# Kernel optimization log

Measured on AMD Instinct MI355X. Metric: run time of the kernel, lower is better.

Reference implementation:

```python
import jax, jax.numpy as jnp
import numpy as np

IN_CHANNELS = 256
OUT_CHANNELS = 256
KERNEL_SIZE = 3
CHANNELS_PER_FILTER = 32
B, H, W = 4, 56, 56


def setup_inputs() -> dict:
    key = jax.random.key(0)
    k1, k2, k3 = jax.random.split(key, 3)
    x = jax.random.normal(k1, (B, IN_CHANNELS, H, W), dtype=jnp.float32)
    # kaiming-uniform-ish scale: bound = 1/sqrt(fan_in)
    fan_in = CHANNELS_PER_FILTER * KERNEL_SIZE ** 2
    bound = 1.0 / np.sqrt(fan_in)
    weight = jax.random.uniform(
        k2, (OUT_CHANNELS, CHANNELS_PER_FILTER, KERNEL_SIZE, KERNEL_SIZE),
        dtype=jnp.float32, minval=-bound, maxval=bound)
    connections = jax.random.randint(
        k3, (OUT_CHANNELS, CHANNELS_PER_FILTER), 0, IN_CHANNELS, dtype=jnp.int32)
    return {"x": x, "weight": weight, "connections": connections}


def reference(x, weight, connections):
    # x: (B, Cin, H, W); weight: (O, cpf, k, k); connections: (O, cpf) int32
    B_, O, cpf = x.shape[0], weight.shape[0], weight.shape[1]
    Hh, Ww = x.shape[2], x.shape[3]
    # Gather each filter's input-channel subset: (B, O, cpf, H, W)
    gathered = x[:, connections]
    # Grouped conv: each of the O groups convolves its cpf channels.
    gathered = gathered.reshape(B_, O * cpf, Hh, Ww)
    out = jax.lax.conv_general_dilated(
        gathered, weight,
        window_strides=(1, 1), padding="SAME",
        dimension_numbers=("NCHW", "OIHW", "NCHW"),
        feature_group_count=O)
    return out  # (B, O, H, W)
```

## Files before the change

kernel.cpp:

```cpp
#include <hip/hip_runtime.h>
#include <stdint.h>

#define NPIX 3136
#define OC 256
#define IC 256
#define CPF 32
#define BUF_FLOATS 3456
#define ZROW 3360

typedef const __attribute__((address_space(1))) uint32_t* gptr_t;
typedef __attribute__((address_space(3))) uint32_t* lptr_t;

__device__ __forceinline__ float dpp_shr1(float v) {
    return __int_as_float(__builtin_amdgcn_update_dpp(
        0, __float_as_int(v), 0x111, 0xF, 0xF, true));
}
__device__ __forceinline__ float dpp_shl1(float v) {
    return __int_as_float(__builtin_amdgcn_update_dpp(
        0, __float_as_int(v), 0x101, 0xF, 0xF, true));
}

__global__ __launch_bounds__(256, 4) void sparse_conv_kernel(
    const float* __restrict__ x, const float* __restrict__ weight,
    const int* __restrict__ connections, float* __restrict__ out)
{
    __shared__ __align__(16) float buf[2][BUF_FLOATS];
    __shared__ __align__(16) float wlds[CPF * 12];
    __shared__ int clds[CPF];

    const int bid = blockIdx.x;
    const int b = bid & 3;
    const int o = bid >> 2;
    const int t = threadIdx.x;
    const int lane = t & 63;
    const int wv = t >> 6;

    if (t < 64) { buf[0][ZROW + t] = 0.f; buf[1][ZROW + t] = 0.f; }

    {
        const float* wo = weight + o * CPF * 9;
        for (int i = t; i < CPF * 9; i += 256) {
            int c = i / 9, k = i - c * 9;
            wlds[c * 12 + k] = wo[i];
        }
        if (t < CPF) clds[t] = connections[o * CPF + t];
    }

    const int cbase = (wv == 0) ? 0 : (3 * wv + 1);
    const int cnum  = (wv == 0) ? 4 : 3;
    int goffs[4], coffs[4];
#pragma unroll
    for (int i = 0; i < 4; ++i) {
        const int chunk = cbase + i;
        int go = chunk * 256 + lane * 4;
        goffs[i] = (go > 3132) ? 3132 : go;
        coffs[i] = chunk * 256;
    }

    const float* xb = x + (size_t)b * IC * NPIX;
    const int s = t & 15;
    const int g = t >> 4;
    const bool active = (g < 14);

    int ro[6];
#pragma unroll
    for (int k = 0; k < 6; ++k) {
        const int rr = 4 * g - 1 + k;
        ro[k] = (((unsigned)rr < 56u) ? rr * 56 : ZROW) + 4 * s;
    }

    float4 acc[4];
#pragma unroll
    for (int r = 0; r < 4; ++r) acc[r] = make_float4(0.f, 0.f, 0.f, 0.f);

    __syncthreads();

    auto dma = [&](int c, float* dst) {
        const float* plane = xb + (size_t)clds[c] * NPIX;
        for (int i = 0; i < cnum; ++i)
            __builtin_amdgcn_global_load_lds((gptr_t)(plane + goffs[i]),
                                             (lptr_t)(dst + coffs[i]), 16, 0, 0);
    };

    auto compute = [&](const float* base, int c) {
        const float4* wp = reinterpret_cast<const float4*>(&wlds[c * 12]);
        const float4 wa = wp[0], wb = wp[1], wc = wp[2];
        const float wt[9] = {wa.x, wa.y, wa.z, wa.w, wb.x, wb.y, wb.z, wb.w, wc.x};
        if (active) {
#pragma unroll
            for (int k = 0; k < 6; ++k) {
                const float4 m = *reinterpret_cast<const float4*>(base + ro[k]);
                const float L = dpp_shr1(m.w);
                float       R = dpp_shl1(m.x);
                R = (s == 13) ? 0.f : R;
#pragma unroll
                for (int r = 0; r < 4; ++r) {
                    const int kh = k - r;
                    if (kh >= 0 && kh < 3) {
                        const float w0 = wt[kh * 3 + 0];
                        const float w1 = wt[kh * 3 + 1];
                        const float w2 = wt[kh * 3 + 2];
                        acc[r].x += w0 * L    + w1 * m.x + w2 * m.y;
                        acc[r].y += w0 * m.x  + w1 * m.y + w2 * m.z;
                        acc[r].z += w0 * m.y  + w1 * m.z + w2 * m.w;
                        acc[r].w += w0 * m.z  + w1 * m.w + w2 * R;
                    }
                }
            }
        }
    };

    dma(0, &buf[0][0]);
    __syncthreads();

#pragma unroll 1
    for (int it = 0; it < 16; ++it) {
        const int c = 2 * it;
        dma(c + 1, &buf[1][0]);
        compute(&buf[0][0], c);
        __syncthreads();
        if (it < 15) dma(c + 2, &buf[0][0]);
        compute(&buf[1][0], c + 1);
        __syncthreads();
    }

    if (active && s < 14) {
        float* ob = out + ((size_t)b * OC + o) * NPIX + (4 * g) * 56 + 4 * s;
#pragma unroll
        for (int r = 0; r < 4; ++r)
            *reinterpret_cast<float4*>(ob + r * 56) = acc[r];
    }
}

extern "C" void kernel_launch(void* const* d_in, const int* in_sizes, int n_in,
                              void* d_out, int out_size, void* d_ws, size_t ws_size,
                              hipStream_t stream) {
    const float* x    = (const float*)d_in[0];
    const float* wgt  = (const float*)d_in[1];
    const int*   conn = (const int*)d_in[2];
    float* out = (float*)d_out;

    dim3 grid(4 * OC);
    dim3 block(256);
    hipLaunchKernelGGL(sparse_conv_kernel, grid, block, 0, stream, x, wgt, conn, out);
}
```

Measured before the change: 122.2 us.

## Split each output plane into two row halves to double blocks and occupancy

Each block now computes half of an output plane (28 rows), so the grid doubles to 2048 blocks and LDS per block shrinks, allowing launch bounds of 8 blocks per CU. Each thread computes 2 output rows instead of 4, with a 29-row halo window loaded per channel. Weights and connection indices are read directly from global memory instead of being staged in LDS. The aim is more parallelism and latency hiding, at the cost of extra halo loads (29 of 56 rows per half) and less per-thread reuse of loaded rows.

```diff
diff --git a/kernel.cpp b/kernel.cpp
--- a/kernel.cpp
+++ b/kernel.cpp
@@ -5,8 +5,10 @@
 #define OC 256
 #define IC 256
 #define CPF 32
-#define BUF_FLOATS 3456
-#define ZROW 3360
+#define BUFSZ 1856
+#define ZROW 1792
+#define WLEN 1624
+#define CLAMP 1620
 
 typedef const __attribute__((address_space(1))) uint32_t* gptr_t;
 typedef __attribute__((address_space(3))) uint32_t* lptr_t;
@@ -20,81 +22,78 @@
         0, __float_as_int(v), 0x101, 0xF, 0xF, true));
 }
 
-__global__ __launch_bounds__(256, 4) void sparse_conv_kernel(
+__global__ __launch_bounds__(256, 8) void sparse_conv_kernel(
     const float* __restrict__ x, const float* __restrict__ weight,
     const int* __restrict__ connections, float* __restrict__ out)
 {
-    __shared__ __align__(16) float buf[2][BUF_FLOATS];
-    __shared__ __align__(16) float wlds[CPF * 12];
-    __shared__ int clds[CPF];
+    __shared__ __align__(16) float buf[2][BUFSZ];
 
-    const int bid = blockIdx.x;
-    const int b = bid & 3;
-    const int o = bid >> 2;
-    const int t = threadIdx.x;
+    const int bid  = blockIdx.x;
+    const int half = bid & 1;
+    const int b    = (bid >> 1) & 3;
+    const int o    = bid >> 3;
+    const int t    = threadIdx.x;
     const int lane = t & 63;
-    const int wv = t >> 6;
+    const int wv   = t >> 6;
 
     if (t < 64) { buf[0][ZROW + t] = 0.f; buf[1][ZROW + t] = 0.f; }
 
-    {
-        const float* wo = weight + o * CPF * 9;
-        for (int i = t; i < CPF * 9; i += 256) {
-            int c = i / 9, k = i - c * 9;
-            wlds[c * 12 + k] = wo[i];
-        }
-        if (t < CPF) clds[t] = connections[o * CPF + t];
-    }
+    const int r0 = half * 28;
+    const int rs = half ? 27 : 0;
 
-    const int cbase = (wv == 0) ? 0 : (3 * wv + 1);
-    const int cnum  = (wv == 0) ? 4 : 3;
-    int goffs[4], coffs[4];
+    const int cnum = (wv == 3) ? 1 : 2;
+    int goffs[2], coffs[2];
 #pragma unroll
-    for (int i = 0; i < 4; ++i) {
-        const int chunk = cbase + i;
+    for (int i = 0; i < 2; ++i) {
+        const int chunk = wv + 4 * i;
         int go = chunk * 256 + lane * 4;
-        goffs[i] = (go > 3132) ? 3132 : go;
+        goffs[i] = (go > CLAMP) ? CLAMP : go;
         coffs[i] = chunk * 256;
     }
 
-    const float* xb = x + (size_t)b * IC * NPIX;
+    const float* xb   = x + (size_t)b * IC * NPIX + rs * 56;
+    const int*   conn = connections + o * CPF;
+    const float* wo   = weight + o * CPF * 9;
+
     const int s = t & 15;
     const int g = t >> 4;
     const bool active = (g < 14);
 
-    int ro[6];
+    int ro[4];
 #pragma unroll
-    for (int k = 0; k < 6; ++k) {
-        const int rr = 4 * g - 1 + k;
-        ro[k] = (((unsigned)rr < 56u) ? rr * 56 : ZROW) + 4 * s;
+    for (int k = 0; k < 4; ++k) {
+        const int rr = r0 + 2 * g - 1 + k;
+        const unsigned lr = (unsigned)(rr - rs);
+        ro[k] = ((lr <= 28u) ? (int)lr * 56 : ZROW) + 4 * s;
     }
 
-    float4 acc[4];
-#pragma unroll
-    for (int r = 0; r < 4; ++r) acc[r] = make_float4(0.f, 0.f, 0.f, 0.f);
+    float4 acc[2];
+    acc[0] = make_float4(0.f, 0.f, 0.f, 0.f);
+    acc[1] = make_float4(0.f, 0.f, 0.f, 0.f);
 
     __syncthreads();
 
     auto dma = [&](int c, float* dst) {
-        const float* plane = xb + (size_t)clds[c] * NPIX;
+        const float* plane = xb + (size_t)conn[c] * NPIX;
         for (int i = 0; i < cnum; ++i)
             __builtin_amdgcn_global_load_lds((gptr_t)(plane + goffs[i]),
                                              (lptr_t)(dst + coffs[i]), 16, 0, 0);
     };
 
     auto compute = [&](const float* base, int c) {
-        const float4* wp = reinterpret_cast<const float4*>(&wlds[c * 12]);
-        const float4 wa = wp[0], wb = wp[1], wc = wp[2];
-        const float wt[9] = {wa.x, wa.y, wa.z, wa.w, wb.x, wb.y, wb.z, wb.w, wc.x};
+        const float* wp = wo + c * 9;
+        float wt[9];
+#pragma unroll
+        for (int k = 0; k < 9; ++k) wt[k] = wp[k];
         if (active) {
 #pragma unroll
-            for (int k = 0; k < 6; ++k) {
+            for (int k = 0; k < 4; ++k) {
                 const float4 m = *reinterpret_cast<const float4*>(base + ro[k]);
                 const float L = dpp_shr1(m.w);
                 float       R = dpp_shl1(m.x);
                 R = (s == 13) ? 0.f : R;
 #pragma unroll
-                for (int r = 0; r < 4; ++r) {
+                for (int r = 0; r < 2; ++r) {
                     const int kh = k - r;
                     if (kh >= 0 && kh < 3) {
                         const float w0 = wt[kh * 3 + 0];
@@ -125,10 +124,9 @@
     }
 
     if (active && s < 14) {
-        float* ob = out + ((size_t)b * OC + o) * NPIX + (4 * g) * 56 + 4 * s;
-#pragma unroll
-        for (int r = 0; r < 4; ++r)
-            *reinterpret_cast<float4*>(ob + r * 56) = acc[r];
+        float* ob = out + ((size_t)b * OC + o) * NPIX + (r0 + 2 * g) * 56 + 4 * s;
+        *reinterpret_cast<float4*>(ob)      = acc[0];
+        *reinterpret_cast<float4*>(ob + 56) = acc[1];
     }
 }
 
@@ -140,7 +138,7 @@
     const int*   conn = (const int*)d_in[2];
     float* out = (float*)d_out;
 
-    dim3 grid(4 * OC);
+    dim3 grid(8 * OC);
     dim3 block(256);
     hipLaunchKernelGGL(sparse_conv_kernel, grid, block, 0, stream, x, wgt, conn, out);
 }
```

Measured after the change: 116.3 us. 4.8% less time.
